# Kernel tuning notes

Measured on AMD Instinct MI355X. Metric: run time of the kernel, lower is better.

Reference implementation:

```python
import jax, jax.numpy as jnp
import numpy as np

NUM_JOINT_LIST = [8, 10, 12, 14, 16, 18, 20, 22, 24, 9, 13, 17]
NUM_GLOBAL_LIST = [1, 0, 1, 1, 0, 1, 1, 1, 0, 1, 1, 1]
M = len(NUM_JOINT_LIST)
B, T, JMAX = 16, 128, 24
H, HEADS, L, RANK = 256, 8, 4, 8
DH = H // HEADS
LAYERSCALE = 1e-4


def setup_inputs():
    key = jax.random.key(0)
    ks = jax.random.split(key, 40)
    m_idx = jax.random.randint(ks[0], (B,), 0, M)
    nj = jnp.array(NUM_JOINT_LIST)[m_idx]
    valid = jnp.arange(JMAX)[None, :] < nj[:, None]  # (B, J) real joints of each morphology
    jtype = jax.random.randint(ks[1], (B, JMAX), 0, 3)  # 0 slide, 1 hinge, 2 global
    has_g = (jnp.array(NUM_GLOBAL_LIST) > 0)[m_idx][:, None]
    jtype = jnp.where((jtype == 2) & ~has_g, 0, jtype)
    tile = lambda m: jnp.broadcast_to(m[:, None, :], (B, T, JMAX))
    slide_mask = tile((jtype == 0) & valid)
    hinge_mask = tile((jtype == 1) & valid)
    global_mask = tile((jtype == 2) & valid)
    act_mask = tile(valid)
    morph_mask = (valid[:, :, None] & valid[:, None, :]) | jnp.eye(JMAX, dtype=bool)[None]
    act = jax.random.normal(ks[2], (B, T, JMAX, 1), dtype=jnp.float32)
    s = 0.02
    inp = dict(act=act, slide_mask=slide_mask, hinge_mask=hinge_mask,
               global_mask=global_mask, act_mask=act_mask, morph_mask=morph_mask,
               m_idx=m_idx)
    inp['Ws'] = s * jax.random.normal(ks[3], (1, H)); inp['bs'] = jnp.zeros((H,))
    inp['Wh'] = s * jax.random.normal(ks[4], (1, H)); inp['bh'] = jnp.zeros((H,))
    inp['Wg'] = s * jax.random.normal(ks[5], (M, H))
    inp['Wact'] = s * jax.random.normal(ks[6], (1, H))
    pos = jax.random.normal(ks[7], (M, JMAX, H))
    pos_valid = jnp.arange(JMAX)[None, :, None] < jnp.array(NUM_JOINT_LIST)[:, None, None]
    inp['pos'] = pos * pos_valid  # rows beyond num_joint stay zero, as in the torch loop
    inp['ln1_s'] = jnp.ones((L, H)); inp['ln1_b'] = jnp.zeros((L, H))
    inp['Wqkv'] = s * jax.random.normal(ks[8], (L, H, 3 * H)); inp['bqkv'] = jnp.zeros((L, 3 * H))
    inp['loraA'] = s * jax.random.normal(ks[9], (L, M, H, RANK))
    inp['loraB'] = s * jax.random.normal(ks[10], (L, M, RANK, 3 * H))
    inp['Wo'] = s * jax.random.normal(ks[11], (L, H, H)); inp['bo'] = jnp.zeros((L, H))
    inp['ln2_s'] = jnp.ones((L, H)); inp['ln2_b'] = jnp.zeros((L, H))
    inp['W1'] = s * jax.random.normal(ks[12], (L, H, 4 * H)); inp['b1'] = jnp.zeros((L, 4 * H))
    inp['W2'] = s * jax.random.normal(ks[13], (L, 4 * H, H)); inp['b2'] = jnp.zeros((L, H))
    inp['g1'] = LAYERSCALE * jnp.ones((L, H)); inp['g2'] = LAYERSCALE * jnp.ones((L, H))
    inp['lnf_s'] = jnp.ones((H,)); inp['lnf_b'] = jnp.zeros((H,))
    return inp


def _ln(z, sc, bi):
    mu = z.mean(-1, keepdims=True)
    v = ((z - mu) ** 2).mean(-1, keepdims=True)
    return (z - mu) * jax.lax.rsqrt(v + 1e-5) * sc + bi


def reference(act, slide_mask, hinge_mask, global_mask, act_mask, morph_mask, m_idx,
              Ws, bs, Wh, bh, Wg, Wact, pos,
              ln1_s, ln1_b, Wqkv, bqkv, loraA, loraB, Wo, bo,
              ln2_s, ln2_b, W1, b1, W2, b2, g1, g2, lnf_s, lnf_b):
    has_g = (jnp.array(NUM_GLOBAL_LIST) > 0)[m_idx]  # (B,)
    a1 = act[..., :1]  # slide_dim = hinge_dim = num_global = 1
    emb = jnp.where(slide_mask[..., None], a1 @ Ws + bs, jnp.zeros((), act.dtype))
    emb = jnp.where(hinge_mask[..., None], a1 @ Wh + bh, emb)
    emb_g = a1 * Wg[m_idx][:, None, None, :]  # per-sample morphology-routed projection
    emb = jnp.where((global_mask & has_g[:, None, None])[..., None], emb_g, emb)
    y = emb + act_mask[..., None].astype(emb.dtype) * Wact[0]
    y = y + pos[m_idx][:, None]  # (B, T, J, H)
    Bv, Tv, J, _ = y.shape
    N = Bv * Tv
    x = y.reshape(N, J, H)
    amask = jnp.broadcast_to(morph_mask[:, None], (Bv, Tv, J, J)).reshape(N, J, J)
    t_idx = jnp.repeat(m_idx, Tv)  # (N,)
    neg = jnp.finfo(x.dtype).min
    scale = 1.0 / np.sqrt(DH)

    def block(x, lp):
        l1s, l1b, wqkv, bq, lA, lB, wo, bo_, l2s, l2b, w1, b1_, w2, b2_, gg1, gg2 = lp
        h = _ln(x, l1s, l1b)
        qkv = h @ wqkv + bq
        # per-task LoRA on qkv, gathered by morphology index
        qkv = qkv + jnp.einsum('njr,nrk->njk', jnp.einsum('njd,ndr->njr', h, lA[t_idx]), lB[t_idx])
        q, k, v = jnp.split(qkv, 3, axis=-1)
        q = q.reshape(N, J, HEADS, DH).transpose(0, 2, 1, 3)
        k = k.reshape(N, J, HEADS, DH).transpose(0, 2, 1, 3)
        v = v.reshape(N, J, HEADS, DH).transpose(0, 2, 1, 3)
        scores = jnp.einsum('nhid,nhjd->nhij', q, k) * scale
        scores = jnp.where(amask[:, None], scores, neg)
        attn = jax.nn.softmax(scores, axis=-1)
        o = jnp.einsum('nhij,nhjd->nhid', attn, v).transpose(0, 2, 1, 3).reshape(N, J, H)
        x = x + gg1 * (o @ wo + bo_)
        h2 = _ln(x, l2s, l2b)
        x = x + gg2 * (jax.nn.gelu(h2 @ w1 + b1_) @ w2 + b2_)
        return x, None

    x, _ = jax.lax.scan(block, x, (ln1_s, ln1_b, Wqkv, bqkv, loraA, loraB, Wo, bo,
                                   ln2_s, ln2_b, W1, b1, W2, b2, g1, g2))
    x = _ln(x, lnf_s, lnf_b)
    return x.reshape(Bv, Tv, J, H)
```

## Files before the change

### kernel.cpp

```cpp
#include <hip/hip_runtime.h>
#include <cstdint>
#include <cstddef>

#define B_     16
#define T_     128
#define J_     24
#define H_     256
#define HEADS_ 8
#define DH_    32
#define L_     4
#define RANK_  8
#define M_     12
#define NTOK   (B_*T_)
#define ROWS   (NTOK*J_)
#define KQ     320
#define HAS_G_MASK 3821

typedef __attribute__((ext_vector_type(8))) short short8;
typedef __attribute__((ext_vector_type(4))) float f32x4;

__constant__ int cNJ[M_] = {8, 10, 12, 14, 16, 18, 20, 22, 24, 9, 13, 17};

__device__ __forceinline__ float bf2f(unsigned short u) {
    union { unsigned int i; float f; } c; c.i = ((unsigned int)u) << 16; return c.f;
}
__device__ __forceinline__ unsigned short f2bf(float f) {
    union { float f; unsigned int i; } c; c.f = f;
    unsigned int x = c.i;
    return (unsigned short)((x + 0x7fffu + ((x >> 16) & 1u)) >> 16);
}
__device__ __forceinline__ float asf(unsigned int u) {
    union { unsigned int i; float f; } c; c.i = u; return c.f;
}
__device__ __forceinline__ unsigned int cvtpk(float lo, float hi) {
    unsigned int r;
    asm("v_cvt_pk_bf16_f32 %0, %1, %2" : "=v"(r) : "v"(lo), "v"(hi));
    return r;
}
__device__ __forceinline__ void gload16(const void* g, void* l) {
    __builtin_amdgcn_global_load_lds((const __attribute__((address_space(1))) void*)g,
                                     (__attribute__((address_space(3))) void*)l, 16, 0, 0);
}
#define SWZ(r) ((((r) >> 1) & 3) << 4)

__global__ void zero_flag(int* f) { *f = 0; }

__global__ __launch_bounds__(256) void detect_kernel(
    const unsigned char* __restrict__ sl, const unsigned char* __restrict__ hi,
    const unsigned char* __restrict__ gl, const int* __restrict__ m_idx,
    int* __restrict__ flag) {
    int rj = blockIdx.x * 256 + threadIdx.x;
    if (rj >= ROWS) return;
    int b = rj / (T_ * J_);
    int j = rj % J_;
    int valid = (j < cNJ[m_idx[b]]) ? 1 : 0;
    int cnt = (sl[rj] != 0) + (hi[rj] != 0) + (gl[rj] != 0);
    if (cnt != valid) atomicOr(flag, 1);
}

__global__ void wconv_t(const float* __restrict__ W, unsigned short* __restrict__ WT,
                        int K, int Nc, int total) {
    int i = blockIdx.x * 256 + threadIdx.x;
    if (i >= total) return;
    int kn = K * Nc;
    int l = i / kn;
    int r = i - l * kn;
    int n = r / K;
    int k = r - n * K;
    WT[i] = f2bf(W[(size_t)l * kn + (size_t)k * Nc + n]);
}

__global__ void wconv_qkv(const float* __restrict__ Wqkv, const float* __restrict__ loraB,
                          unsigned short* __restrict__ OT) {
    int i = blockIdx.x * 256 + threadIdx.x;
    const int total = L_ * M_ * 768 * KQ;
    if (i >= total) return;
    int k = i % KQ;
    int n = (i / KQ) % 768;
    int m = (i / (KQ * 768)) % M_;
    int l = i / (KQ * 768 * M_);
    float v = 0.f;
    if (k < 256)      v = Wqkv[((size_t)l * 256 + k) * 768 + n];
    else if (k < 264) v = loraB[(((size_t)l * M_ + m) * RANK_ + (k - 256)) * 768 + n];
    OT[i] = f2bf(v);
}

__global__ __launch_bounds__(256) void embed_ln_kernel(
    const float* __restrict__ act, const void* __restrict__ slide,
    const void* __restrict__ hinge, const void* __restrict__ glob,
    const int* __restrict__ m_idx, const int* __restrict__ flag,
    const float* __restrict__ Ws, const float* __restrict__ bs,
    const float* __restrict__ Wh, const float* __restrict__ bh,
    const float* __restrict__ Wg, const float* __restrict__ Wact,
    const float* __restrict__ pos, const float* __restrict__ lns,
    const float* __restrict__ lnb, const float* __restrict__ lA,
    float* __restrict__ X, unsigned short* __restrict__ Hq) {
    int rj = (blockIdx.x << 2) + (threadIdx.x >> 6);
    int lane = threadIdx.x & 63;
    int b = rj / (T_ * J_);
    int j = rj % J_;
    int m = m_idx[b];
    bool valid = j < cNJ[m];
    bool s, hh, gl;
    if (*flag) {
        s  = ((const int*)slide)[rj] != 0;
        hh = ((const int*)hinge)[rj] != 0;
        gl = ((const int*)glob)[rj]  != 0;
    } else {
        s  = ((const unsigned char*)slide)[rj] != 0;
        hh = ((const unsigned char*)hinge)[rj] != 0;
        gl = ((const unsigned char*)glob)[rj]  != 0;
    }
    float a1 = act[rj];
    int h0 = lane << 2;
    float e0 = 0.f, e1 = 0.f, e2 = 0.f, e3 = 0.f;
    if (s) {
        float4 w = *(const float4*)(Ws + h0); float4 bb = *(const float4*)(bs + h0);
        e0 = a1 * w.x + bb.x; e1 = a1 * w.y + bb.y; e2 = a1 * w.z + bb.z; e3 = a1 * w.w + bb.w;
    } else if (hh) {
        float4 w = *(const float4*)(Wh + h0); float4 bb = *(const float4*)(bh + h0);
        e0 = a1 * w.x + bb.x; e1 = a1 * w.y + bb.y; e2 = a1 * w.z + bb.z; e3 = a1 * w.w + bb.w;
    } else if (gl && ((HAS_G_MASK >> m) & 1)) {
        float4 w = *(const float4*)(Wg + m * H_ + h0);
        e0 = a1 * w.x; e1 = a1 * w.y; e2 = a1 * w.z; e3 = a1 * w.w;
    }
    if (valid) {
        float4 wa = *(const float4*)(Wact + h0);
        e0 += wa.x; e1 += wa.y; e2 += wa.z; e3 += wa.w;
    }
    float4 pv = *(const float4*)(pos + (size_t)(m * J_ + j) * H_ + h0);
    float y0 = e0 + pv.x, y1 = e1 + pv.y, y2 = e2 + pv.z, y3 = e3 + pv.w;
    float4 out; out.x = y0; out.y = y1; out.z = y2; out.w = y3;
    *(float4*)(X + ((size_t)rj << 8) + h0) = out;

    float s1 = y0 + y1 + y2 + y3;
    float s2 = y0 * y0 + y1 * y1 + y2 * y2 + y3 * y3;
    #pragma unroll
    for (int o = 32; o; o >>= 1) { s1 += __shfl_xor(s1, o); s2 += __shfl_xor(s2, o); }
    float mu = s1 * (1.f / H_);
    float var = s2 * (1.f / H_) - mu * mu;
    float rs = rsqrtf(var + 1e-5f);
    float4 scv = *(const float4*)(lns + h0);
    float4 biv = *(const float4*)(lnb + h0);
    float hn0 = (y0 - mu) * rs * scv.x + biv.x;
    float hn1 = (y1 - mu) * rs * scv.y + biv.y;
    float hn2 = (y2 - mu) * rs * scv.z + biv.z;
    float hn3 = (y3 - mu) * rs * scv.w + biv.w;
    ushort4 o4; o4.x = f2bf(hn0); o4.y = f2bf(hn1); o4.z = f2bf(hn2); o4.w = f2bf(hn3);
    *(ushort4*)(Hq + (size_t)rj * KQ + h0) = o4;

    int t = m;
    const float* Ap = lA + (size_t)t * (H_ * RANK_) + h0 * RANK_;
    float4 av[8];
    #pragma unroll
    for (int c = 0; c < 8; ++c) av[c] = ((const float4*)Ap)[c];
    float hn[4] = {hn0, hn1, hn2, hn3};
    float p[RANK_];
    #pragma unroll
    for (int k = 0; k < RANK_; ++k) p[k] = 0.f;
    #pragma unroll
    for (int i = 0; i < 4; ++i)
        #pragma unroll
        for (int k = 0; k < RANK_; ++k) {
            int idx = i * RANK_ + k;
            float a = (idx & 3) == 0 ? av[idx >> 2].x : (idx & 3) == 1 ? av[idx >> 2].y
                    : (idx & 3) == 2 ? av[idx >> 2].z : av[idx >> 2].w;
            p[k] += hn[i] * a;
        }
    #pragma unroll
    for (int k = 0; k < RANK_; ++k)
        #pragma unroll
        for (int o = 32; o; o >>= 1) p[k] += __shfl_xor(p[k], o);
    unsigned int w0 = (unsigned int)f2bf(p[0]) | ((unsigned int)f2bf(p[1]) << 16);
    unsigned int w1 = (unsigned int)f2bf(p[2]) | ((unsigned int)f2bf(p[3]) << 16);
    unsigned int w2 = (unsigned int)f2bf(p[4]) | ((unsigned int)f2bf(p[5]) << 16);
    unsigned int w3 = (unsigned int)f2bf(p[6]) | ((unsigned int)f2bf(p[7]) << 16);
    unsigned int tv = 0;
    if (lane == 0) tv = w0; else if (lane == 1) tv = w1;
    else if (lane == 2) tv = w2; else if (lane == 3) tv = w3;
    if (lane < 32)
        *((unsigned int*)(Hq + (size_t)rj * KQ + 256) + lane) = tv;
}

__global__ __launch_bounds__(256) void lora_tail_kernel(
    unsigned short* __restrict__ Hq, const float* __restrict__ lA,
    const int* __restrict__ m_idx) {
    int row = (blockIdx.x << 2) + (threadIdx.x >> 6);
    int lane = threadIdx.x & 63;
    int t = m_idx[row / (J_ * T_)];
    int h0 = lane << 2;
    ushort4 hv = *(const ushort4*)(Hq + (size_t)row * KQ + h0);
    float hn[4] = {bf2f(hv.x), bf2f(hv.y), bf2f(hv.z), bf2f(hv.w)};
    const float* Ap = lA + (size_t)t * (H_ * RANK_) + h0 * RANK_;
    float4 av[8];
    #pragma unroll
    for (int c = 0; c < 8; ++c) av[c] = ((const float4*)Ap)[c];
    float p[RANK_];
    #pragma unroll
    for (int k = 0; k < RANK_; ++k) p[k] = 0.f;
    #pragma unroll
    for (int i = 0; i < 4; ++i)
        #pragma unroll
        for (int k = 0; k < RANK_; ++k) {
            int idx = i * RANK_ + k;
            float a = (idx & 3) == 0 ? av[idx >> 2].x : (idx & 3) == 1 ? av[idx >> 2].y
                    : (idx & 3) == 2 ? av[idx >> 2].z : av[idx >> 2].w;
            p[k] += hn[i] * a;
        }
    #pragma unroll
    for (int k = 0; k < RANK_; ++k)
        #pragma unroll
        for (int o = 32; o; o >>= 1) p[k] += __shfl_xor(p[k], o);
    unsigned int w0 = (unsigned int)f2bf(p[0]) | ((unsigned int)f2bf(p[1]) << 16);
    unsigned int w1 = (unsigned int)f2bf(p[2]) | ((unsigned int)f2bf(p[3]) << 16);
    unsigned int w2 = (unsigned int)f2bf(p[4]) | ((unsigned int)f2bf(p[5]) << 16);
    unsigned int w3 = (unsigned int)f2bf(p[6]) | ((unsigned int)f2bf(p[7]) << 16);
    unsigned int tv = 0;
    if (lane == 0) tv = w0; else if (lane == 1) tv = w1;
    else if (lane == 2) tv = w2; else if (lane == 3) tv = w3;
    if (lane < 32)
        *((unsigned int*)(Hq + (size_t)row * KQ + 256) + lane) = tv;
}

template<int EPI, int K, int NC>
__global__ __launch_bounds__(256) void gemm_k(
    const unsigned short* __restrict__ A, const unsigned short* __restrict__ BT,
    const float* __restrict__ bias, const int* __restrict__ m_idx,
    unsigned short* __restrict__ outB) {
    __shared__ __align__(16) char LAs[2][8192];
    __shared__ __align__(16) char LBs[2][8192];
    char* LA0 = &LAs[0][0]; char* LA1 = &LAs[1][0];
    char* LB0 = &LBs[0][0]; char* LB1 = &LBs[1][0];
    int gx = gridDim.x;
    int nwg = gx * gridDim.y;
    int id = blockIdx.y * gx + blockIdx.x;
    int q8 = nwg >> 3;
    int sid = (id & 7) * q8 + (id >> 3);
    int bx = sid % gx, by = sid / gx;
    int col0 = bx * 128;
    int row0 = by * 128;
    int tid = threadIdx.x;
    int wv = tid >> 6, lane = tid & 63;
    int wm = wv >> 1, wn = wv & 1;

    const unsigned short* BTe = BT;
    if (EPI == 0) BTe += (size_t)m_idx[row0 / (J_ * T_)] * (768 * KQ);

    int srow  = tid >> 2;
    int sbyte = (tid & 3) << 4;
    int sce   = (sbyte ^ SWZ(srow)) >> 1;
    const unsigned short* Ab = A   + (size_t)(row0 + srow) * K + sce;
    const unsigned short* Bb = BTe + (size_t)(col0 + srow) * K + sce;
    const size_t rstep = (size_t)64 * K;

    int rdoff = ((lane >> 4) << 4) ^ SWZ(lane & 15);
    int rowA0 = wm * 64 + (lane & 15);
    int rowB0 = wn * 64 + (lane & 15);

    f32x4 acc[4][4];
    const f32x4 z = {0.f, 0.f, 0.f, 0.f};
    #pragma unroll
    for (int mi = 0; mi < 4; ++mi)
        #pragma unroll
        for (int ni = 0; ni < 4; ++ni) acc[mi][ni] = z;

    constexpr int NT = K >> 5;

    auto STAGE = [&](int kt, int b) {
        const unsigned short* a = Ab + (kt << 5);
        const unsigned short* bb = Bb + (kt << 5);
        char* la = (b ? LA1 : LA0) + (tid << 4);
        char* lb = (b ? LB1 : LB0) + (tid << 4);
        gload16(a, la);          gload16(a + rstep, la + 4096);
        gload16(bb, lb);         gload16(bb + rstep, lb + 4096);
    };
    auto COMPUTE = [&](const char* pa, const char* pb) {
        short8 af[4], bfr[4];
        #pragma unroll
        for (int q = 0; q < 4; ++q) {
            af[q]  = *(const short8*)(pa + (rowA0 + q * 16) * 64 + rdoff);
            bfr[q] = *(const short8*)(pb + (rowB0 + q * 16) * 64 + rdoff);
        }
        #pragma unroll
        for (int mi = 0; mi < 4; ++mi)
            #pragma unroll
            for (int ni = 0; ni < 4; ++ni)
                acc[mi][ni] = __builtin_amdgcn_mfma_f32_16x16x32_bf16(bfr[ni], af[mi], acc[mi][ni], 0, 0, 0);
    };

    STAGE(0, 0);
    for (int t = 0; t < NT; t += 2) {
        if (t + 1 < NT) { STAGE(t + 1, 1); asm volatile("s_waitcnt vmcnt(4)" ::: "memory"); }
        else            { asm volatile("s_waitcnt vmcnt(0)" ::: "memory"); }
        __builtin_amdgcn_s_barrier();
        __builtin_amdgcn_sched_barrier(0);
        COMPUTE(LA0, LB0);
        __builtin_amdgcn_sched_barrier(0);
        __builtin_amdgcn_s_barrier();
        if (t + 2 < NT) { STAGE(t + 2, 0); asm volatile("s_waitcnt vmcnt(4)" ::: "memory"); }
        else            { asm volatile("s_waitcnt vmcnt(0)" ::: "memory"); }
        __builtin_amdgcn_s_barrier();
        __builtin_amdgcn_sched_barrier(0);
        COMPUTE(LA1, LB1);
        __builtin_amdgcn_sched_barrier(0);
        __builtin_amdgcn_s_barrier();
    }

    int rb = row0 + wm * 64 + (lane & 15);
    int cb = col0 + wn * 64 + ((lane >> 4) << 2);

    #pragma unroll
    for (int mi = 0; mi < 4; ++mi) {
        int row = rb + mi * 16;
        #pragma unroll
        for (int ni = 0; ni < 4; ++ni) {
            int col = cb + ni * 16;
            float4 bv = *(const float4*)(bias + col);
            float v[4] = {acc[mi][ni][0] + bv.x, acc[mi][ni][1] + bv.y,
                          acc[mi][ni][2] + bv.z, acc[mi][ni][3] + bv.w};
            if (EPI == 1) {
                #pragma unroll
                for (int r = 0; r < 4; ++r) {
                    float u = v[r];
                    float tt = u * u;
                    float pp = fmaf(tt, 0.044715f, 1.0f) * u;
                    float e = exp2f(-2.3025850929940457f * pp);
                    v[r] = u / (1.f + e);
                }
            }
            uint2 st; st.x = cvtpk(v[0], v[1]); st.y = cvtpk(v[2], v[3]);
            *(uint2*)(outB + (size_t)row * NC + col) = st;
        }
    }
}

template<int MODE, int K>
__global__ __launch_bounds__(256) void resid_gemm(
    const unsigned short* __restrict__ A, const unsigned short* __restrict__ BT,
    const float* __restrict__ bias, const float* __restrict__ gv,
    float* __restrict__ X, unsigned short* __restrict__ Hout,
    const float* __restrict__ lns, const float* __restrict__ lnb) {
    __shared__ __align__(16) char LAs[2][4096];
    __shared__ __align__(16) char LBs[2][16384];
    __shared__ float red1[4][16][4], red2[4][16][4];
    char* LA0 = &LAs[0][0]; char* LA1 = &LAs[1][0];
    char* LB0 = &LBs[0][0]; char* LB1 = &LBs[1][0];
    int nwg = gridDim.x;
    int id = blockIdx.x;
    int q8 = nwg >> 3;
    int sid = (id & 7) * q8 + (id >> 3);
    int row0 = sid * 64;
    int tid = threadIdx.x;
    int wn = tid >> 6, lane = tid & 63;

    int srow  = tid >> 2;
    int sbyte = (tid & 3) << 4;
    int sce   = (sbyte ^ SWZ(srow)) >> 1;
    const unsigned short* Ab = A  + (size_t)(row0 + srow) * K + sce;
    const unsigned short* Bb = BT + (size_t)srow * K + sce;
    const size_t bstep = (size_t)64 * K;

    int rdoff = ((lane >> 4) << 4) ^ SWZ(lane & 15);
    int rowB0 = wn * 64 + (lane & 15);

    f32x4 acc[4][4];
    const f32x4 z = {0.f, 0.f, 0.f, 0.f};
    #pragma unroll
    for (int mi = 0; mi < 4; ++mi)
        #pragma unroll
        for (int ni = 0; ni < 4; ++ni) acc[mi][ni] = z;

    constexpr int NT = K >> 5;

    auto STAGE = [&](int kt, int b) {
        const unsigned short* a = Ab + (kt << 5);
        const unsigned short* bb = Bb + (kt << 5);
        char* la = (b ? LA1 : LA0) + (tid << 4);
        char* lb = (b ? LB1 : LB0) + (tid << 4);
        gload16(a, la);
        gload16(bb,             lb);
        gload16(bb + bstep,     lb + 4096);
        gload16(bb + 2 * bstep, lb + 8192);
        gload16(bb + 3 * bstep, lb + 12288);
    };
    auto COMPUTE = [&](const char* pa, const char* pb) {
        short8 af[4], bfr[4];
        #pragma unroll
        for (int q = 0; q < 4; ++q) {
            af[q]  = *(const short8*)(pa + ((lane & 15) + q * 16) * 64 + rdoff);
            bfr[q] = *(const short8*)(pb + (rowB0 + q * 16) * 64 + rdoff);
        }
        #pragma unroll
        for (int mi = 0; mi < 4; ++mi)
            #pragma unroll
            for (int ni = 0; ni < 4; ++ni)
                acc[mi][ni] = __builtin_amdgcn_mfma_f32_16x16x32_bf16(bfr[ni], af[mi], acc[mi][ni], 0, 0, 0);
    };

    STAGE(0, 0);
    for (int t = 0; t < NT; t += 2) {
        if (t + 1 < NT) { STAGE(t + 1, 1); asm volatile("s_waitcnt vmcnt(5)" ::: "memory"); }
        else            { asm volatile("s_waitcnt vmcnt(0)" ::: "memory"); }
        __builtin_amdgcn_s_barrier();
        __builtin_amdgcn_sched_barrier(0);
        COMPUTE(LA0, LB0);
        __builtin_amdgcn_sched_barrier(0);
        __builtin_amdgcn_s_barrier();
        if (t + 2 < NT) { STAGE(t + 2, 0); asm volatile("s_waitcnt vmcnt(5)" ::: "memory"); }
        else            { asm volatile("s_waitcnt vmcnt(0)" ::: "memory"); }
        __builtin_amdgcn_s_barrier();
        __builtin_amdgcn_sched_barrier(0);
        COMPUTE(LA1, LB1);
        __builtin_amdgcn_sched_barrier(0);
        __builtin_amdgcn_s_barrier();
    }

    int rb0 = row0 + (lane & 15);
    int cb = (wn << 6) + ((lane >> 4) << 2);
    float4 b4[4], g4[4];
    #pragma unroll
    for (int ni = 0; ni < 4; ++ni) {
        b4[ni] = *(const float4*)(bias + cb + ni * 16);
        g4[ni] = *(const float4*)(gv + cb + ni * 16);
    }
    float s1[4] = {0, 0, 0, 0}, s2[4] = {0, 0, 0, 0};
    #pragma unroll
    for (int mi = 0; mi < 4; ++mi) {
        int row = rb0 + mi * 16;
        #pragma unroll
        for (int ni = 0; ni < 4; ++ni) {
            int col = cb + ni * 16;
            float4 x = *(const float4*)(X + ((size_t)row << 8) + col);
            float u0 = fmaf(g4[ni].x, acc[mi][ni][0] + b4[ni].x, x.x);
            float u1 = fmaf(g4[ni].y, acc[mi][ni][1] + b4[ni].y, x.y);
            float u2 = fmaf(g4[ni].z, acc[mi][ni][2] + b4[ni].z, x.z);
            float u3 = fmaf(g4[ni].w, acc[mi][ni][3] + b4[ni].w, x.w);
            if (MODE != 2) {
                float4 st; st.x = u0; st.y = u1; st.z = u2; st.w = u3;
                *(float4*)(X + ((size_t)row << 8) + col) = st;
            }
            acc[mi][ni][0] = u0; acc[mi][ni][1] = u1;
            acc[mi][ni][2] = u2; acc[mi][ni][3] = u3;
            s1[mi] += u0 + u1 + u2 + u3;
            s2[mi] += u0 * u0 + u1 * u1 + u2 * u2 + u3 * u3;
        }
    }
    #pragma unroll
    for (int mi = 0; mi < 4; ++mi) {
        s1[mi] += __shfl_xor(s1[mi], 16); s1[mi] += __shfl_xor(s1[mi], 32);
        s2[mi] += __shfl_xor(s2[mi], 16); s2[mi] += __shfl_xor(s2[mi], 32);
    }
    if (lane < 16) {
        #pragma unroll
        for (int mi = 0; mi < 4; ++mi) { red1[mi][lane][wn] = s1[mi]; red2[mi][lane][wn] = s2[mi]; }
    }
    __syncthreads();
    float mu[4], rs[4];
    #pragma unroll
    for (int mi = 0; mi < 4; ++mi) {
        int r = lane & 15;
        float t1 = red1[mi][r][0] + red1[mi][r][1] + red1[mi][r][2] + red1[mi][r][3];
        float t2 = red2[mi][r][0] + red2[mi][r][1] + red2[mi][r][2] + red2[mi][r][3];
        mu[mi] = t1 * (1.f / H_);
        float var = t2 * (1.f / H_) - mu[mi] * mu[mi];
        rs[mi] = rsqrtf(var + 1e-5f);
    }
    float4 l4[4], o4v[4];
    #pragma unroll
    for (int ni = 0; ni < 4; ++ni) {
        l4[ni]  = *(const float4*)(lns + cb + ni * 16);
        o4v[ni] = *(const float4*)(lnb + cb + ni * 16);
    }
    #pragma unroll
    for (int mi = 0; mi < 4; ++mi) {
        int row = rb0 + mi * 16;
        #pragma unroll
        for (int ni = 0; ni < 4; ++ni) {
            int col = cb + ni * 16;
            float h0 = (acc[mi][ni][0] - mu[mi]) * rs[mi] * l4[ni].x + o4v[ni].x;
            float h1 = (acc[mi][ni][1] - mu[mi]) * rs[mi] * l4[ni].y + o4v[ni].y;
            float h2 = (acc[mi][ni][2] - mu[mi]) * rs[mi] * l4[ni].z + o4v[ni].z;
            float h3 = (acc[mi][ni][3] - mu[mi]) * rs[mi] * l4[ni].w + o4v[ni].w;
            if (MODE == 2) {
                float4 st; st.x = h0; st.y = h1; st.z = h2; st.w = h3;
                *(float4*)(X + ((size_t)row << 8) + col) = st;
            } else {
                constexpr int ldh = (MODE == 1) ? KQ : H_;
                uint2 st; st.x = cvtpk(h0, h1); st.y = cvtpk(h2, h3);
                *(uint2*)(Hout + (size_t)row * ldh + col) = st;
            }
        }
    }
}

__global__ __launch_bounds__(256) void attn_kernel(
    const unsigned short* __restrict__ QKV, const int* __restrict__ m_idx,
    unsigned short* __restrict__ O) {
    __shared__ unsigned int q2s[4][24][18];
    __shared__ unsigned int k2s[4][16][26];
    __shared__ unsigned int v2s[4][24][18];
    __shared__ float       scs[4][24][27];
    int w = threadIdx.x >> 6, lane = threadIdx.x & 63;
    int n = blockIdx.x >> 1;
    int hd = ((blockIdx.x & 1) << 2) + w;
    int nj = cNJ[m_idx[n >> 7]];
    unsigned int (*q2)[18] = q2s[w];
    unsigned int (*k2)[26] = k2s[w];
    unsigned int (*v2)[18] = v2s[w];
    float (*sc)[27] = scs[w];

    const unsigned short* base = QKV + (size_t)n * (J_ * 768) + hd * DH_;

    #pragma unroll
    for (int it = 0; it < 3; ++it) {
        int r = it * 64 + lane;
        int j = r >> 3, d0 = (r & 7) << 2, d2 = d0 >> 1;
        ushort4 x = *(const ushort4*)(base + (size_t)j * 768 + d0);
        q2[j][d2]     = (unsigned int)x.x | ((unsigned int)x.y << 16);
        q2[j][d2 + 1] = (unsigned int)x.z | ((unsigned int)x.w << 16);
    }
    #pragma unroll
    for (int it = 0; it < 3; ++it) {
        int r = it * 64 + lane;
        int j = r >> 3, d0 = (r & 7) << 2, d2 = d0 >> 1;
        ushort4 x = *(const ushort4*)(base + (size_t)j * 768 + 256 + d0);
        k2[d2][j]     = (unsigned int)x.x | ((unsigned int)x.y << 16);
        k2[d2 + 1][j] = (unsigned int)x.z | ((unsigned int)x.w << 16);
    }
    #pragma unroll
    for (int it = 0; it < 3; ++it) {
        int r = it * 64 + lane;
        int j = r >> 3, d0 = (r & 7) << 2, d2 = d0 >> 1;
        ushort4 x = *(const ushort4*)(base + (size_t)j * 768 + 512 + d0);
        v2[j][d2]     = (unsigned int)x.x | ((unsigned int)x.y << 16);
        v2[j][d2 + 1] = (unsigned int)x.z | ((unsigned int)x.w << 16);
    }

    int i = lane >> 1, half = lane & 1;
    if (lane < 48) {
        float qf[32];
        #pragma unroll
        for (int d2 = 0; d2 < 16; ++d2) {
            unsigned int x = q2[i][d2];
            qf[2 * d2]     = asf(x << 16);
            qf[2 * d2 + 1] = asf(x & 0xffff0000u);
        }
        int jb = half * 12;
        float s[12];
        #pragma unroll
        for (int jj = 0; jj < 12; ++jj) {
            int j = jb + jj;
            float acc = 0.f;
            #pragma unroll
            for (int d2 = 0; d2 < 16; ++d2) {
                unsigned int x = k2[d2][j];
                acc += qf[2 * d2] * asf(x << 16);
                acc += qf[2 * d2 + 1] * asf(x & 0xffff0000u);
            }
            bool ok = (i < nj && j < nj) || (i == j);
            s[jj] = ok ? acc * 0.17677669529663687f : -1e30f;
        }
        float mx = s[0];
        #pragma unroll
        for (int jj = 1; jj < 12; ++jj) mx = fmaxf(mx, s[jj]);
        mx = fmaxf(mx, __shfl_xor(mx, 1));
        float sm = 0.f;
        #pragma unroll
        for (int jj = 0; jj < 12; ++jj) { float e = __expf(s[jj] - mx); s[jj] = e; sm += e; }
        sm += __shfl_xor(sm, 1);
        float inv = 1.f / sm;
        #pragma unroll
        for (int jj = 0; jj < 12; ++jj) sc[i][jb + jj] = s[jj] * inv;
    }

    #pragma unroll
    for (int it = 0; it < 6; ++it) {
        int i2 = it * 4 + (lane >> 4), d2 = lane & 15;
        float olo = 0.f, ohi = 0.f;
        #pragma unroll
        for (int j = 0; j < J_; ++j) {
            float p = sc[i2][j];
            unsigned int x = v2[j][d2];
            olo += p * asf(x << 16);
            ohi += p * asf(x & 0xffff0000u);
        }
        unsigned int o = (unsigned int)f2bf(olo) | ((unsigned int)f2bf(ohi) << 16);
        *(unsigned int*)(O + (size_t)(n * J_ + i2) * H_ + hd * DH_ + 2 * d2) = o;
    }
}

extern "C" void kernel_launch(void* const* d_in, const int* in_sizes, int n_in,
                              void* d_out, int out_size, void* d_ws, size_t ws_size,
                              hipStream_t stream) {
    (void)in_sizes; (void)n_in; (void)out_size; (void)ws_size;
    const float* act   = (const float*)d_in[0];
    const void*  slide = d_in[1];
    const void*  hinge = d_in[2];
    const void*  glob  = d_in[3];
    const int* m_idx  = (const int*)d_in[6];
    const float* Ws   = (const float*)d_in[7];
    const float* bs   = (const float*)d_in[8];
    const float* Wh   = (const float*)d_in[9];
    const float* bh   = (const float*)d_in[10];
    const float* Wg   = (const float*)d_in[11];
    const float* Wact = (const float*)d_in[12];
    const float* pos  = (const float*)d_in[13];
    const float* ln1s = (const float*)d_in[14];
    const float* ln1b = (const float*)d_in[15];
    const float* Wqkv = (const float*)d_in[16];
    const float* bqkv = (const float*)d_in[17];
    const float* loraA= (const float*)d_in[18];
    const float* loraB= (const float*)d_in[19];
    const float* Wo   = (const float*)d_in[20];
    const float* bo   = (const float*)d_in[21];
    const float* ln2s = (const float*)d_in[22];
    const float* ln2b = (const float*)d_in[23];
    const float* W1   = (const float*)d_in[24];
    const float* b1   = (const float*)d_in[25];
    const float* W2   = (const float*)d_in[26];
    const float* b2   = (const float*)d_in[27];
    const float* g1   = (const float*)d_in[28];
    const float* g2   = (const float*)d_in[29];
    const float* lnfs = (const float*)d_in[30];
    const float* lnfb = (const float*)d_in[31];

    float* X = (float*)d_out;

    size_t off = 0;
    char* ws = (char*)d_ws;
    auto nxt = [&](size_t bytes) -> char* {
        char* p = ws + off; off += (bytes + 255) & ~(size_t)255; return p;
    };
    int*            dflag  = (int*)nxt(256);
    unsigned short* Hq     = (unsigned short*)nxt((size_t)ROWS * KQ * 2);
    unsigned short* Hw     = (unsigned short*)nxt((size_t)ROWS * H_ * 2);
    unsigned short* QKVG   = (unsigned short*)nxt((size_t)ROWS * 1024 * 2);
    unsigned short* WqkvTp = (unsigned short*)nxt((size_t)L_ * M_ * 768 * KQ * 2);
    unsigned short* WoT    = (unsigned short*)nxt((size_t)L_ * H_ * H_ * 2);
    unsigned short* W1T    = (unsigned short*)nxt((size_t)L_ * H_ * 1024 * 2);
    unsigned short* W2T    = (unsigned short*)nxt((size_t)L_ * 1024 * H_ * 2);
    unsigned short* Obf    = Hq;

    zero_flag<<<1, 1, 0, stream>>>(dflag);
    detect_kernel<<<(ROWS + 255) / 256, 256, 0, stream>>>(
        (const unsigned char*)slide, (const unsigned char*)hinge,
        (const unsigned char*)glob, m_idx, dflag);

    wconv_qkv<<<(L_ * M_ * 768 * KQ + 255) / 256, 256, 0, stream>>>(Wqkv, loraB, WqkvTp);
    wconv_t<<<(L_ * H_ * H_   + 255) / 256, 256, 0, stream>>>(Wo, WoT, H_, H_,   L_ * H_ * H_);
    wconv_t<<<(L_ * H_ * 1024 + 255) / 256, 256, 0, stream>>>(W1, W1T, H_, 1024, L_ * H_ * 1024);
    wconv_t<<<(L_ * 1024 * H_ + 255) / 256, 256, 0, stream>>>(W2, W2T, 1024, H_, L_ * 1024 * H_);

    embed_ln_kernel<<<ROWS / 4, 256, 0, stream>>>(act, slide, hinge, glob, m_idx, dflag,
                                                  Ws, bs, Wh, bh, Wg, Wact, pos,
                                                  ln1s, ln1b, loraA, X, Hq);

    for (int l = 0; l < L_; ++l) {
        gemm_k<0, KQ, 768><<<dim3(6, 384), 256, 0, stream>>>(
            Hq, WqkvTp + (size_t)l * M_ * 768 * KQ, bqkv + l * 768, m_idx, QKVG);
        attn_kernel<<<NTOK * 2, 256, 0, stream>>>(QKVG, m_idx, Obf);
        resid_gemm<0, 256><<<768, 256, 0, stream>>>(
            Obf, WoT + (size_t)l * H_ * H_, bo + l * H_, g1 + l * H_,
            X, Hw, ln2s + l * H_, ln2b + l * H_);
        gemm_k<1, 256, 1024><<<dim3(8, 384), 256, 0, stream>>>(
            Hw, W1T + (size_t)l * H_ * 1024, b1 + l * 1024, m_idx, QKVG);
        if (l < L_ - 1) {
            resid_gemm<1, 1024><<<768, 256, 0, stream>>>(
                QKVG, W2T + (size_t)l * 1024 * H_, b2 + l * H_, g2 + l * H_,
                X, Hq, ln1s + (l + 1) * H_, ln1b + (l + 1) * H_);
            lora_tail_kernel<<<ROWS / 4, 256, 0, stream>>>(
                Hq, loraA + (size_t)(l + 1) * M_ * H_ * RANK_, m_idx);
        } else {
            resid_gemm<2, 1024><<<768, 256, 0, stream>>>(
                QKVG, W2T + (size_t)l * 1024 * H_, b2 + l * H_, g2 + l * H_,
                X, nullptr, lnfs, lnfb);
        }
    }
}
```

Baseline: 1.374 ms.

## Overlap global prefetch with MFMA compute and enlarge residual GEMM tiles to 128 rows

The GEMM main loops now issue the next tile's global-to-LDS loads and immediately compute on the current buffer, waiting for the loads only after compute. This replaces the old wait-then-compute ordering and drops one barrier per half-step. The residual GEMM also moves to 512-thread blocks covering 128 rows, so each loaded weight tile is reused by two row groups, and the LayerNorm reduction is extended across the extra wave dimension. The cost is fewer blocks in flight (half the grid, launch bounds forcing one block per SIMD group) and a full vmcnt(0) drain every step instead of partial waits.

```diff
diff --git a/kernel.cpp b/kernel.cpp
--- a/kernel.cpp
+++ b/kernel.cpp
@@ -289,21 +289,24 @@
     };
 
     STAGE(0, 0);
+    asm volatile("s_waitcnt vmcnt(0)" ::: "memory");
+    __builtin_amdgcn_s_barrier();
+    __builtin_amdgcn_sched_barrier(0);
     for (int t = 0; t < NT; t += 2) {
-        if (t + 1 < NT) { STAGE(t + 1, 1); asm volatile("s_waitcnt vmcnt(4)" ::: "memory"); }
-        else            { asm volatile("s_waitcnt vmcnt(0)" ::: "memory"); }
+        STAGE(t + 1, 1);
+        COMPUTE(LA0, LB0);
+        __builtin_amdgcn_sched_barrier(0);
+        asm volatile("s_waitcnt vmcnt(0)" ::: "memory");
         __builtin_amdgcn_s_barrier();
         __builtin_amdgcn_sched_barrier(0);
-        COMPUTE(LA0, LB0);
-        __builtin_amdgcn_sched_barrier(0);
-        __builtin_amdgcn_s_barrier();
-        if (t + 2 < NT) { STAGE(t + 2, 0); asm volatile("s_waitcnt vmcnt(4)" ::: "memory"); }
-        else            { asm volatile("s_waitcnt vmcnt(0)" ::: "memory"); }
-        __builtin_amdgcn_s_barrier();
-        __builtin_amdgcn_sched_barrier(0);
+        if (t + 2 < NT) STAGE(t + 2, 0);
         COMPUTE(LA1, LB1);
-        __builtin_amdgcn_sched_barrier(0);
-        __builtin_amdgcn_s_barrier();
+        if (t + 2 < NT) {
+            __builtin_amdgcn_sched_barrier(0);
+            asm volatile("s_waitcnt vmcnt(0)" ::: "memory");
+            __builtin_amdgcn_s_barrier();
+            __builtin_amdgcn_sched_barrier(0);
+        }
     }
 
     int rb = row0 + wm * 64 + (lane & 15);
@@ -335,32 +338,34 @@
 }
 
 template<int MODE, int K>
-__global__ __launch_bounds__(256) void resid_gemm(
+__global__ __launch_bounds__(512, 1) void resid_gemm(
     const unsigned short* __restrict__ A, const unsigned short* __restrict__ BT,
     const float* __restrict__ bias, const float* __restrict__ gv,
     float* __restrict__ X, unsigned short* __restrict__ Hout,
     const float* __restrict__ lns, const float* __restrict__ lnb) {
-    __shared__ __align__(16) char LAs[2][4096];
+    __shared__ __align__(16) char LAs[2][8192];
     __shared__ __align__(16) char LBs[2][16384];
-    __shared__ float red1[4][16][4], red2[4][16][4];
+    __shared__ float red1[4][16][2][4], red2[4][16][2][4];
     char* LA0 = &LAs[0][0]; char* LA1 = &LAs[1][0];
     char* LB0 = &LBs[0][0]; char* LB1 = &LBs[1][0];
     int nwg = gridDim.x;
     int id = blockIdx.x;
     int q8 = nwg >> 3;
     int sid = (id & 7) * q8 + (id >> 3);
-    int row0 = sid * 64;
+    int row0 = sid * 128;
     int tid = threadIdx.x;
-    int wn = tid >> 6, lane = tid & 63;
-
-    int srow  = tid >> 2;
-    int sbyte = (tid & 3) << 4;
-    int sce   = (sbyte ^ SWZ(srow)) >> 1;
-    const unsigned short* Ab = A  + (size_t)(row0 + srow) * K + sce;
-    const unsigned short* Bb = BT + (size_t)srow * K + sce;
-    const size_t bstep = (size_t)64 * K;
+    int wv = tid >> 6, lane = tid & 63;
+    int wm = wv >> 2, wn = wv & 3;
+
+    int arow = tid >> 2, aslot = (tid & 3) << 4;
+    const unsigned short* Ab = A + (size_t)(row0 + arow) * K + ((aslot ^ SWZ(arow)) >> 1);
+    int brow0 = tid >> 2,         bslot0 = (tid & 3) << 4;
+    int brow1 = (tid + 512) >> 2, bslot1 = (tid & 3) << 4;
+    const unsigned short* Bb0 = BT + (size_t)brow0 * K + ((bslot0 ^ SWZ(brow0)) >> 1);
+    const unsigned short* Bb1 = BT + (size_t)brow1 * K + ((bslot1 ^ SWZ(brow1)) >> 1);
 
     int rdoff = ((lane >> 4) << 4) ^ SWZ(lane & 15);
+    int rowA0 = wm * 64 + (lane & 15);
     int rowB0 = wn * 64 + (lane & 15);
 
     f32x4 acc[4][4];
@@ -373,21 +378,17 @@
     constexpr int NT = K >> 5;
 
     auto STAGE = [&](int kt, int b) {
-        const unsigned short* a = Ab + (kt << 5);
-        const unsigned short* bb = Bb + (kt << 5);
         char* la = (b ? LA1 : LA0) + (tid << 4);
         char* lb = (b ? LB1 : LB0) + (tid << 4);
-        gload16(a, la);
-        gload16(bb,             lb);
-        gload16(bb + bstep,     lb + 4096);
-        gload16(bb + 2 * bstep, lb + 8192);
-        gload16(bb + 3 * bstep, lb + 12288);
+        gload16(Ab + (kt << 5),  la);
+        gload16(Bb0 + (kt << 5), lb);
+        gload16(Bb1 + (kt << 5), lb + 8192);
     };
     auto COMPUTE = [&](const char* pa, const char* pb) {
         short8 af[4], bfr[4];
         #pragma unroll
         for (int q = 0; q < 4; ++q) {
-            af[q]  = *(const short8*)(pa + ((lane & 15) + q * 16) * 64 + rdoff);
+            af[q]  = *(const short8*)(pa + (rowA0 + q * 16) * 64 + rdoff);
             bfr[q] = *(const short8*)(pb + (rowB0 + q * 16) * 64 + rdoff);
         }
         #pragma unroll
@@ -398,24 +399,27 @@
     };
 
     STAGE(0, 0);
+    asm volatile("s_waitcnt vmcnt(0)" ::: "memory");
+    __builtin_amdgcn_s_barrier();
+    __builtin_amdgcn_sched_barrier(0);
     for (int t = 0; t < NT; t += 2) {
-        if (t + 1 < NT) { STAGE(t + 1, 1); asm volatile("s_waitcnt vmcnt(5)" ::: "memory"); }
-        else            { asm volatile("s_waitcnt vmcnt(0)" ::: "memory"); }
+        STAGE(t + 1, 1);
+        COMPUTE(LA0, LB0);
+        __builtin_amdgcn_sched_barrier(0);
+        asm volatile("s_waitcnt vmcnt(0)" ::: "memory");
         __builtin_amdgcn_s_barrier();
         __builtin_amdgcn_sched_barrier(0);
-        COMPUTE(LA0, LB0);
-        __builtin_amdgcn_sched_barrier(0);
-        __builtin_amdgcn_s_barrier();
-        if (t + 2 < NT) { STAGE(t + 2, 0); asm volatile("s_waitcnt vmcnt(5)" ::: "memory"); }
-        else            { asm volatile("s_waitcnt vmcnt(0)" ::: "memory"); }
-        __builtin_amdgcn_s_barrier();
-        __builtin_amdgcn_sched_barrier(0);
+        if (t + 2 < NT) STAGE(t + 2, 0);
         COMPUTE(LA1, LB1);
-        __builtin_amdgcn_sched_barrier(0);
-        __builtin_amdgcn_s_barrier();
-    }
-
-    int rb0 = row0 + (lane & 15);
+        if (t + 2 < NT) {
+            __builtin_amdgcn_sched_barrier(0);
+            asm volatile("s_waitcnt vmcnt(0)" ::: "memory");
+            __builtin_amdgcn_s_barrier();
+            __builtin_amdgcn_sched_barrier(0);
+        }
+    }
+
+    int rb0 = row0 + wm * 64 + (lane & 15);
     int cb = (wn << 6) + ((lane >> 4) << 2);
     float4 b4[4], g4[4];
     #pragma unroll
@@ -450,17 +454,21 @@
         s1[mi] += __shfl_xor(s1[mi], 16); s1[mi] += __shfl_xor(s1[mi], 32);
         s2[mi] += __shfl_xor(s2[mi], 16); s2[mi] += __shfl_xor(s2[mi], 32);
     }
+    __syncthreads();
     if (lane < 16) {
         #pragma unroll
-        for (int mi = 0; mi < 4; ++mi) { red1[mi][lane][wn] = s1[mi]; red2[mi][lane][wn] = s2[mi]; }
+        for (int mi = 0; mi < 4; ++mi) {
+            red1[mi][lane][wm][wn] = s1[mi];
+            red2[mi][lane][wm][wn] = s2[mi];
+        }
     }
     __syncthreads();
     float mu[4], rs[4];
     #pragma unroll
     for (int mi = 0; mi < 4; ++mi) {
         int r = lane & 15;
-        float t1 = red1[mi][r][0] + red1[mi][r][1] + red1[mi][r][2] + red1[mi][r][3];
-        float t2 = red2[mi][r][0] + red2[mi][r][1] + red2[mi][r][2] + red2[mi][r][3];
+        float t1 = red1[mi][r][wm][0] + red1[mi][r][wm][1] + red1[mi][r][wm][2] + red1[mi][r][wm][3];
+        float t2 = red2[mi][r][wm][0] + red2[mi][r][wm][1] + red2[mi][r][wm][2] + red2[mi][r][wm][3];
         mu[mi] = t1 * (1.f / H_);
         float var = t2 * (1.f / H_) - mu[mi] * mu[mi];
         rs[mi] = rsqrtf(var + 1e-5f);
@@ -659,19 +667,19 @@
         gemm_k<0, KQ, 768><<<dim3(6, 384), 256, 0, stream>>>(
             Hq, WqkvTp + (size_t)l * M_ * 768 * KQ, bqkv + l * 768, m_idx, QKVG);
         attn_kernel<<<NTOK * 2, 256, 0, stream>>>(QKVG, m_idx, Obf);
-        resid_gemm<0, 256><<<768, 256, 0, stream>>>(
+        resid_gemm<0, 256><<<384, 512, 0, stream>>>(
             Obf, WoT + (size_t)l * H_ * H_, bo + l * H_, g1 + l * H_,
             X, Hw, ln2s + l * H_, ln2b + l * H_);
         gemm_k<1, 256, 1024><<<dim3(8, 384), 256, 0, stream>>>(
             Hw, W1T + (size_t)l * H_ * 1024, b1 + l * 1024, m_idx, QKVG);
         if (l < L_ - 1) {
-            resid_gemm<1, 1024><<<768, 256, 0, stream>>>(
+            resid_gemm<1, 1024><<<384, 512, 0, stream>>>(
                 QKVG, W2T + (size_t)l * 1024 * H_, b2 + l * H_, g2 + l * H_,
                 X, Hq, ln1s + (l + 1) * H_, ln1b + (l + 1) * H_);
             lora_tail_kernel<<<ROWS / 4, 256, 0, stream>>>(
                 Hq, loraA + (size_t)(l + 1) * M_ * H_ * RANK_, m_idx);
         } else {
-            resid_gemm<2, 1024><<<768, 256, 0, stream>>>(
+            resid_gemm<2, 1024><<<384, 512, 0, stream>>>(
                 QKVG, W2T + (size_t)l * 1024 * H_, b2 + l * H_, g2 + l * H_,
                 X, nullptr, lnfs, lnfb);
         }
```

Result: slower. 1.462 ms (+6.4%).
